# Optimization experiments

Measured on AMD Instinct MI355X. Metric: run time of the kernel, lower is better.

The kernel has to match this reference:

```python
import jax, jax.numpy as jnp
import numpy as np

N = 50000       # nodes
E = 800000      # edges
F_IN = 128      # dataset.num_node_features
H = 128         # hidden_channels (all equal), pool_dim
FC1, FC2 = 512, 256
G = 512         # number of graphs
C = 32          # dataset.num_classes
EPS = 1e-5      # BatchNorm eps


def setup_inputs() -> dict:
    key = jax.random.key(0)
    ks = jax.random.split(key, 16)
    rn = lambda k, s: jax.random.normal(k, s, jnp.float32) * 0.05
    return {
        "x": jax.random.normal(ks[0], (N, F_IN), jnp.float32),
        "edge_index": jax.random.randint(ks[1], (2, E), 0, N),
        "batch": jnp.sort(jax.random.randint(ks[2], (N,), 0, G)),
        "W1": rn(ks[3], (F_IN, H)), "b1": jnp.zeros((H,), jnp.float32),
        "W2": rn(ks[4], (H, H)),    "b2": jnp.zeros((H,), jnp.float32),
        "W3": rn(ks[5], (H, H)),    "b3": jnp.zeros((H,), jnp.float32),
        "W4": rn(ks[6], (H, H)),    "b4": jnp.zeros((H,), jnp.float32),
        "lw1": rn(ks[7], (H, FC1)),   "lb1": jnp.zeros((FC1,), jnp.float32),
        "lw2": rn(ks[8], (FC1, FC2)), "lb2": jnp.zeros((FC2,), jnp.float32),
        "lw3": rn(ks[9], (FC2, C)),   "lb3": jnp.zeros((C,), jnp.float32),
        "g1": jnp.ones((FC1,), jnp.float32), "be1": jnp.zeros((FC1,), jnp.float32),
        "g2": jnp.ones((FC2,), jnp.float32), "be2": jnp.zeros((FC2,), jnp.float32),
    }


def _gcn_structure(edge_index):
    # add self loops, then symmetric deg^-1/2 normalization (PyG GCNConv default)
    loop = jnp.arange(N)
    src = jnp.concatenate([edge_index[0], loop])
    dst = jnp.concatenate([edge_index[1], loop])
    deg = jax.ops.segment_sum(jnp.ones_like(src, jnp.float32), dst, num_segments=N)
    dinv = jnp.where(deg > 0, jax.lax.rsqrt(deg), 0.0)
    norm = dinv[src] * dinv[dst]          # [E + N]
    return src, dst, norm


def _gcn_conv(x, src, dst, norm, W, b):
    h = x @ W                              # [N, out]
    agg = jax.ops.segment_sum(h[src] * norm[:, None], dst, num_segments=N)
    return agg + b


def _bn(h, gamma, beta):
    # training-mode batch stats (biased variance), as torch BatchNorm1d
    m = jnp.mean(h, axis=0)
    v = jnp.var(h, axis=0)
    return (h - m) * jax.lax.rsqrt(v + EPS) * gamma + beta


def reference(x, edge_index, batch, W1, b1, W2, b2, W3, b3, W4, b4,
              lw1, lb1, lw2, lb2, lw3, lb3, g1, be1, g2, be2):
    src, dst, norm = _gcn_structure(edge_index)
    x = jax.nn.relu(_gcn_conv(x, src, dst, norm, W1, b1))
    x = jax.nn.relu(_gcn_conv(x, src, dst, norm, W2, b2))
    x = jax.nn.relu(_gcn_conv(x, src, dst, norm, W3, b3))
    x = jax.nn.relu(_gcn_conv(x, src, dst, norm, W4, b4))
    # global_add_pool over graphs
    p = jax.ops.segment_sum(x, batch, num_segments=G)   # [G, H]
    h = jax.nn.relu(p @ lw1 + lb1)
    h = _bn(h, g1, be1)                                  # dropout = identity (eval)
    h = jax.nn.relu(h @ lw2 + lb2)
    h = _bn(h, g2, be2)
    return jax.nn.sigmoid(h @ lw3 + lb3)                 # [G, C]
```

## Files before the change

### kernel.cpp

```cpp
#include <hip/hip_runtime.h>
#include <hip/hip_fp16.h>
#include <math.h>

#define NN 50000
#define NE 800000
#define FT 128
#define NG 512
#define F1 512
#define F2 256
#define NC 32
#define BN_EPS 1e-5f
#define NSLC (NN / 8)
#define NSTRIP ((NE + 2047) / 2048)

typedef __attribute__((ext_vector_type(8))) unsigned short ushort8;
typedef __attribute__((ext_vector_type(8))) _Float16 f16x8;
typedef __attribute__((ext_vector_type(4))) float f32x4;

__device__ __forceinline__ unsigned short f2h(float f) {
  return __half_as_ushort(__float2half(f));
}
__device__ __forceinline__ float h2f(unsigned short h) {
  return __half2float(__ushort_as_half(h));
}


__global__ __launch_bounds__(256) void k_hist(const int* __restrict__ ei, int* __restrict__ cnt8,
                                              unsigned short* __restrict__ rank16) {
  int c = blockIdx.x & 7;
  int e0 = blockIdx.x * 2048 + threadIdx.x * 8;
  if (e0 >= NE) return;
  int* cn = cnt8 + (size_t)c * NN;
  const int* dst = ei + NE;
  int4 a = *(const int4*)&dst[e0];
  int4 b4 = *(const int4*)&dst[e0 + 4];
  int d[8] = {a.x, a.y, a.z, a.w, b4.x, b4.y, b4.z, b4.w};
  ushort8 r;
#pragma unroll
  for (int j = 0; j < 8; ++j) r[j] = (unsigned short)atomicAdd(&cn[d[j]], 1);
  *(ushort8*)&rank16[e0] = r;
}

__global__ __launch_bounds__(256) void k_sum(int* __restrict__ cnt8, int* __restrict__ cnt) {
  int n = blockIdx.x * 256 + threadIdx.x;
  if (n >= NN) return;
  int s = 0;
#pragma unroll
  for (int c = 0; c < 8; ++c) {
    int v = cnt8[(size_t)c * NN + n];
    cnt8[(size_t)c * NN + n] = s;
    s += v;
  }
  cnt[n] = s;
}

__global__ __launch_bounds__(256) void k_dinv(const int* __restrict__ cnt, float* __restrict__ dinv) {
  int i = blockIdx.x * 256 + threadIdx.x;
  if (i < NN) dinv[i] = rsqrtf((float)(cnt[i] + 1));
}

__global__ __launch_bounds__(256) void k_scan1(const int* __restrict__ cnt, int* __restrict__ bsum) {
  __shared__ int s[256];
  int t = threadIdx.x, i = blockIdx.x * 256 + t;
  s[t] = (i < NN) ? cnt[i] : 0;
  __syncthreads();
  for (int d = 128; d > 0; d >>= 1) {
    if (t < d) s[t] += s[t + d];
    __syncthreads();
  }
  if (t == 0) bsum[blockIdx.x] = s[0];
}

__global__ __launch_bounds__(256) void k_scan2(const int* __restrict__ bsum, int* __restrict__ bscan, int nb) {
  __shared__ int s[256];
  int t = threadIdx.x;
  int v = (t < nb) ? bsum[t] : 0;
  s[t] = v; __syncthreads();
  for (int d = 1; d < 256; d <<= 1) {
    int a = (t >= d) ? s[t - d] : 0;
    __syncthreads();
    s[t] += a;
    __syncthreads();
  }
  bscan[t] = s[t] - v;
}

__global__ __launch_bounds__(256) void k_scan3(const int* __restrict__ cnt, const int* __restrict__ bscan,
                                               int* __restrict__ off) {
  __shared__ int s[256];
  int t = threadIdx.x, i = blockIdx.x * 256 + t;
  int v = (i < NN) ? cnt[i] : 0;
  s[t] = v; __syncthreads();
  for (int d = 1; d < 256; d <<= 1) {
    int a = (t >= d) ? s[t - d] : 0;
    __syncthreads();
    s[t] += a;
    __syncthreads();
  }
  int base = bscan[blockIdx.x];
  if (i < NN) off[i] = base + s[t] - v;
  if (i == NN - 1) off[NN] = base + s[t];
}

__global__ __launch_bounds__(256) void k_fill(const int* __restrict__ ei, const int* __restrict__ off,
                                              const int* __restrict__ pre8,
                                              const unsigned short* __restrict__ rank16,
                                              const float* __restrict__ dinv,
                                              unsigned int* __restrict__ ep) {
  int c = blockIdx.x & 7;
  int lo = c * NSLC, hi = lo + NSLC;
  int strip = blockIdx.x >> 3;
  int e0 = strip * 2048 + threadIdx.x * 8;
  if (e0 >= NE) return;
  const int* prec = pre8 + (size_t)(strip & 7) * NN;
  const int* dst = ei + NE;
  int4 da = *(const int4*)&dst[e0];
  int4 db = *(const int4*)&dst[e0 + 4];
  int4 sa = *(const int4*)&ei[e0];
  int4 sb = *(const int4*)&ei[e0 + 4];
  ushort8 rr = *(const ushort8*)&rank16[e0];
  int d[8] = {da.x, da.y, da.z, da.w, db.x, db.y, db.z, db.w};
  int s[8] = {sa.x, sa.y, sa.z, sa.w, sb.x, sb.y, sb.z, sb.w};
#pragma unroll
  for (int j = 0; j < 8; ++j) {
    if (d[j] >= lo && d[j] < hi) {
      int p = off[d[j]] + prec[d[j]] + (int)rr[j];
      float w = dinv[s[j]] * dinv[d[j]];
      ep[p] = (unsigned int)(s[j] & 0xFFFF) | ((unsigned int)f2h(w) << 16);
    }
  }
}


__global__ __launch_bounds__(256) void k_wprep4(const float* __restrict__ W0, const float* __restrict__ W1,
                                                const float* __restrict__ W2, const float* __restrict__ W3,
                                                unsigned short* __restrict__ Wt) {
  int idx = blockIdx.x * 256 + threadIdx.x;
  int l = idx >> 14;
  int r = idx & 16383;
  int c = r >> 7, k = r & 127;
  const float* W = (l == 0) ? W0 : (l == 1) ? W1 : (l == 2) ? W2 : W3;
  int byte = c * 256 + k * 2;
  byte ^= (c & 7) << 4;
  Wt[l * 16384 + (byte >> 1)] = f2h(W[k * FT + c]);
}


template <int FIRST>
__global__ __launch_bounds__(256) void k_gemm_mfma(const float* __restrict__ Xf,
                                                   const unsigned short* __restrict__ Xh,
                                                   const unsigned short* __restrict__ Wt,
                                                   unsigned short* __restrict__ Oc) {
  __shared__ unsigned short sA[64 * 128];
  __shared__ unsigned short sB[128 * 128];
  int t = threadIdx.x;
#pragma unroll
  for (int i = 0; i < 8; ++i) {
    int off = t * 16 + i * 4096;
    *(float4*)((char*)sB + off) = *(const float4*)((const char*)Wt + off);
  }
  {
    int row = t >> 2, k0 = (t & 3) * 32;
    int grow = blockIdx.x * 64 + row;
    if (grow >= NN) grow = NN - 1;
    if (FIRST) {
      const float* xr = Xf + (size_t)grow * FT + k0;
#pragma unroll
      for (int j = 0; j < 4; ++j) {
        float4 v0 = *(const float4*)&xr[j * 8];
        float4 v1 = *(const float4*)&xr[j * 8 + 4];
        ushort8 w;
        w[0] = f2h(v0.x); w[1] = f2h(v0.y); w[2] = f2h(v0.z); w[3] = f2h(v0.w);
        w[4] = f2h(v1.x); w[5] = f2h(v1.y); w[6] = f2h(v1.z); w[7] = f2h(v1.w);
        int byte = row * 256 + (k0 + j * 8) * 2;
        byte ^= (row & 7) << 4;
        *(ushort8*)((char*)sA + byte) = w;
      }
    } else {
#pragma unroll
      for (int j = 0; j < 4; ++j) {
        int k = k0 + j * 8;
        int ch = k >> 5, ko = k & 31;
        ushort8 v = *(const ushort8*)&Xh[((size_t)ch * NN + grow) * 32 + ko];
        int byte = row * 256 + k * 2;
        byte ^= (row & 7) << 4;
        *(ushort8*)((char*)sA + byte) = v;
      }
    }
  }
  __syncthreads();
  int w = t >> 6, l = t & 63;
  int m = l & 15, ks = l >> 4;
  f16x8 a[4];
#pragma unroll
  for (int kk = 0; kk < 4; ++kk) {
    int r = w * 16 + m;
    int byte = r * 256 + (kk * 32 + ks * 8) * 2;
    byte ^= (r & 7) << 4;
    a[kk] = *(const f16x8*)((const char*)sA + byte);
  }
  f32x4 acc[8];
#pragma unroll
  for (int nf = 0; nf < 8; ++nf) acc[nf] = (f32x4){0.f, 0.f, 0.f, 0.f};
#pragma unroll
  for (int nf = 0; nf < 8; ++nf) {
#pragma unroll
    for (int kk = 0; kk < 4; ++kk) {
      int col = nf * 16 + m;
      int byte = col * 256 + (kk * 32 + ks * 8) * 2;
      byte ^= (col & 7) << 4;
      f16x8 b = *(const f16x8*)((const char*)sB + byte);
      acc[nf] = __builtin_amdgcn_mfma_f32_16x16x32_f16(a[kk], b, acc[nf], 0, 0, 0);
    }
  }
  int orow0 = blockIdx.x * 64 + w * 16 + ks * 4;
#pragma unroll
  for (int nf = 0; nf < 8; ++nf) {
    int ch = nf >> 1;
    int co = ((nf & 1) << 4) + m;
#pragma unroll
    for (int r = 0; r < 4; ++r) {
      int orow = orow0 + r;
      if (orow < NN) Oc[((size_t)ch * NN + orow) * 32 + co] = f2h(acc[nf][r]);
    }
  }
}


__global__ __launch_bounds__(256) void k_aggc(const unsigned short* __restrict__ Hc,
                                              const float* __restrict__ dinv,
                                              const int* __restrict__ off, const unsigned int* __restrict__ ep,
                                              const float* __restrict__ bias, unsigned short* __restrict__ O) {
  int c = blockIdx.x & 3;
  int grp = blockIdx.x >> 2;
  int t = threadIdx.x;
  int node = grp * 64 + (t >> 2);
  int l = t & 3;
  if (node >= NN) return;
  const unsigned short* base = Hc + (size_t)c * NN * 32 + l * 8;
  float di = dinv[node];
  float sw = di * di;
  float acc[8];
  {
    ushort8 sv = *(const ushort8*)&base[(size_t)node * 32];
#pragma unroll
    for (int i = 0; i < 8; ++i) acc[i] = h2f(sv[i]) * sw;
  }
  int e0 = off[node], e1 = off[node + 1];
  int e = e0;
  for (; e + 8 <= e1; e += 8) {
    unsigned int pw[8];
#pragma unroll
    for (int j = 0; j < 8; ++j) pw[j] = ep[e + j];
    ushort8 v[8];
#pragma unroll
    for (int j = 0; j < 8; ++j) v[j] = *(const ushort8*)&base[(size_t)(pw[j] & 0xFFFFu) * 32];
#pragma unroll
    for (int j = 0; j < 8; ++j) {
      float w = h2f((unsigned short)(pw[j] >> 16));
#pragma unroll
      for (int i = 0; i < 8; ++i) acc[i] += h2f(v[j][i]) * w;
    }
  }
  for (; e + 4 <= e1; e += 4) {
    unsigned int p0 = ep[e], p1 = ep[e + 1], p2 = ep[e + 2], p3 = ep[e + 3];
    ushort8 v0 = *(const ushort8*)&base[(size_t)(p0 & 0xFFFFu) * 32];
    ushort8 v1 = *(const ushort8*)&base[(size_t)(p1 & 0xFFFFu) * 32];
    ushort8 v2 = *(const ushort8*)&base[(size_t)(p2 & 0xFFFFu) * 32];
    ushort8 v3 = *(const ushort8*)&base[(size_t)(p3 & 0xFFFFu) * 32];
    float w0 = h2f((unsigned short)(p0 >> 16));
    float w1 = h2f((unsigned short)(p1 >> 16));
    float w2 = h2f((unsigned short)(p2 >> 16));
    float w3 = h2f((unsigned short)(p3 >> 16));
#pragma unroll
    for (int i = 0; i < 8; ++i) acc[i] += h2f(v0[i]) * w0;
#pragma unroll
    for (int i = 0; i < 8; ++i) acc[i] += h2f(v1[i]) * w1;
#pragma unroll
    for (int i = 0; i < 8; ++i) acc[i] += h2f(v2[i]) * w2;
#pragma unroll
    for (int i = 0; i < 8; ++i) acc[i] += h2f(v3[i]) * w3;
  }
  for (; e < e1; ++e) {
    unsigned int pv = ep[e];
    float w = h2f((unsigned short)(pv >> 16));
    ushort8 v = *(const ushort8*)&base[(size_t)(pv & 0xFFFFu) * 32];
#pragma unroll
    for (int i = 0; i < 8; ++i) acc[i] += h2f(v[i]) * w;
  }
  ushort8 outv;
#pragma unroll
  for (int i = 0; i < 8; ++i) {
    float v = acc[i] + bias[c * 32 + l * 8 + i];
    outv[i] = f2h(fmaxf(v, 0.f));
  }
  *(ushort8*)&O[((size_t)c * NN + node) * 32 + l * 8] = outv;
}


__global__ __launch_bounds__(256) void k_bounds(const int* __restrict__ batch, int* __restrict__ gstart,
                                                int* __restrict__ gend) {
  int i = blockIdx.x * 256 + threadIdx.x;
  if (i >= NN) return;
  int b = batch[i];
  if (i == 0 || batch[i - 1] != b) gstart[b] = i;
  if (i == NN - 1 || batch[i + 1] != b) gend[b] = i + 1;
}

__global__ __launch_bounds__(128) void k_pool(const unsigned short* __restrict__ X, const int* __restrict__ gstart,
                                              const int* __restrict__ gend, float* __restrict__ pool) {
  int g = blockIdx.x, t = threadIdx.x;
  int ch = t >> 5, wo = t & 31;
  float s = 0.f;
  int n0 = gstart[g], n1 = gend[g];
  const unsigned short* base = X + (size_t)ch * NN * 32 + wo;
  for (int n = n0; n < n1; ++n) s += h2f(base[(size_t)n * 32]);
  pool[g * FT + t] = s;
}


__global__ __launch_bounds__(256) void k_fc1(const float* __restrict__ P, const float* __restrict__ W,
                                             const float* __restrict__ B, float* __restrict__ O) {
  __shared__ float sp[FT];
  int g = blockIdx.x, t = threadIdx.x;
  if (t < FT) sp[t] = P[g * FT + t];
  __syncthreads();
  float a0 = B[t], a1 = B[t + 256];
  for (int k = 0; k < FT; ++k) {
    float x = sp[k];
    a0 += x * W[k * F1 + t];
    a1 += x * W[k * F1 + t + 256];
  }
  O[g * F1 + t] = fmaxf(a0, 0.f);
  O[g * F1 + t + 256] = fmaxf(a1, 0.f);
}

__global__ __launch_bounds__(256) void k_bnstats(const float* __restrict__ h, int cols,
                                                 float* __restrict__ bm, float* __restrict__ br) {
  __shared__ float ss[256], s2[256];
  int c = blockIdx.x, t = threadIdx.x;
  float a = 0.f, b = 0.f;
  for (int r = t; r < NG; r += 256) {
    float v = h[r * cols + c];
    a += v; b += v * v;
  }
  ss[t] = a; s2[t] = b; __syncthreads();
  for (int d = 128; d > 0; d >>= 1) {
    if (t < d) { ss[t] += ss[t + d]; s2[t] += s2[t + d]; }
    __syncthreads();
  }
  if (t == 0) {
    float m = ss[0] / NG;
    float var = s2[0] / NG - m * m;
    bm[c] = m;
    br[c] = rsqrtf(var + BN_EPS);
  }
}

__global__ __launch_bounds__(256) void k_fc2(const float* __restrict__ H1, const float* __restrict__ bm,
                                             const float* __restrict__ br, const float* __restrict__ gam,
                                             const float* __restrict__ bet, const float* __restrict__ W,
                                             const float* __restrict__ B, float* __restrict__ O) {
  __shared__ float sh[F1];
  int g = blockIdx.x, t = threadIdx.x;
  for (int k = t; k < F1; k += 256) {
    float v = H1[g * F1 + k];
    sh[k] = (v - bm[k]) * br[k] * gam[k] + bet[k];
  }
  __syncthreads();
  float a = B[t];
  for (int k = 0; k < F1; ++k) a += sh[k] * W[k * F2 + t];
  O[g * F2 + t] = fmaxf(a, 0.f);
}

__global__ __launch_bounds__(256) void k_fc3(const float* __restrict__ H2, const float* __restrict__ bm,
                                             const float* __restrict__ br, const float* __restrict__ gam,
                                             const float* __restrict__ bet, const float* __restrict__ W,
                                             const float* __restrict__ B, float* __restrict__ O) {
  __shared__ float sh[F2];
  int g = blockIdx.x, t = threadIdx.x;
  if (t < F2) {
    float v = H2[g * F2 + t];
    sh[t] = (v - bm[t]) * br[t] * gam[t] + bet[t];
  }
  __syncthreads();
  if (t < NC) {
    float a = B[t];
    for (int k = 0; k < F2; ++k) a += sh[k] * W[k * NC + t];
    O[g * NC + t] = 1.f / (1.f + expf(-a));
  }
}


extern "C" void kernel_launch(void* const* d_in, const int* in_sizes, int n_in,
                              void* d_out, int out_size, void* d_ws, size_t ws_size,
                              hipStream_t stream) {
  const float* x     = (const float*)d_in[0];
  const int*   ei    = (const int*)d_in[1];
  const int*   batch = (const int*)d_in[2];
  const float* Wc[4] = {(const float*)d_in[3], (const float*)d_in[5], (const float*)d_in[7], (const float*)d_in[9]};
  const float* Bc[4] = {(const float*)d_in[4], (const float*)d_in[6], (const float*)d_in[8], (const float*)d_in[10]};
  const float* lw1 = (const float*)d_in[11]; const float* lb1 = (const float*)d_in[12];
  const float* lw2 = (const float*)d_in[13]; const float* lb2 = (const float*)d_in[14];
  const float* lw3 = (const float*)d_in[15]; const float* lb3 = (const float*)d_in[16];
  const float* g1  = (const float*)d_in[17]; const float* be1 = (const float*)d_in[18];
  const float* g2  = (const float*)d_in[19]; const float* be2 = (const float*)d_in[20];

  char* p = (char*)d_ws;
  auto take = [&](size_t bytes) {
    char* r = p;
    p += (bytes + 255) & ~(size_t)255;
    return r;
  };
  int*   cnt8   = (int*)take((size_t)8 * NN * 4);
  int*   cnt    = (int*)take((size_t)NN * 4);
  float* dinv   = (float*)take((size_t)NN * 4);
  int*   off    = (int*)take((size_t)(NN + 1) * 4);
  int*   bsum   = (int*)take(256 * 4);
  int*   bscan  = (int*)take(256 * 4);
  int*   gstart = (int*)take((size_t)NG * 4);
  int*   gend   = (int*)take((size_t)NG * 4);
  unsigned short* rank16 = (unsigned short*)take((size_t)NE * 2);
  unsigned int*   ep   = (unsigned int*)take((size_t)NE * 4);
  unsigned short* Wt   = (unsigned short*)take((size_t)4 * FT * FT * 2);
  unsigned short* bufT = (unsigned short*)take((size_t)NN * FT * 2);
  unsigned short* bufA = (unsigned short*)take((size_t)NN * FT * 2);
  unsigned short* bufB = (unsigned short*)take((size_t)NN * FT * 2);
  float* pool   = (float*)take((size_t)NG * FT * 4);
  float* h1     = (float*)take((size_t)NG * F1 * 4);
  float* h2     = (float*)take((size_t)NG * F2 * 4);
  float* bnm1   = (float*)take(F1 * 4);
  float* bnr1   = (float*)take(F1 * 4);
  float* bnm2   = (float*)take(F2 * 4);
  float* bnr2   = (float*)take(F2 * 4);

  const int NB = (NN + 255) / 256;

  hipMemsetAsync(cnt8, 0, (size_t)8 * NN * 4, stream);
  hipMemsetAsync(gstart, 0, (size_t)NG * 4, stream);
  hipMemsetAsync(gend, 0, (size_t)NG * 4, stream);

  k_hist<<<NSTRIP, 256, 0, stream>>>(ei, cnt8, rank16);
  k_sum<<<NB, 256, 0, stream>>>(cnt8, cnt);
  k_dinv<<<NB, 256, 0, stream>>>(cnt, dinv);
  k_scan1<<<NB, 256, 0, stream>>>(cnt, bsum);
  k_scan2<<<1, 256, 0, stream>>>(bsum, bscan, NB);
  k_scan3<<<NB, 256, 0, stream>>>(cnt, bscan, off);
  k_fill<<<NSTRIP * 8, 256, 0, stream>>>(ei, off, cnt8, rank16, dinv, ep);
  k_wprep4<<<256, 256, 0, stream>>>(Wc[0], Wc[1], Wc[2], Wc[3], Wt);

  const int NBLK_G = (NN + 63) / 64;
  const int NGRP_A = (NN + 63) / 64;
  unsigned short* outs[4] = {bufA, bufB, bufA, bufB};
  for (int l = 0; l < 4; ++l) {
    if (l == 0)
      k_gemm_mfma<1><<<NBLK_G, 256, 0, stream>>>(x, (const unsigned short*)nullptr, Wt, bufT);
    else
      k_gemm_mfma<0><<<NBLK_G, 256, 0, stream>>>((const float*)nullptr, outs[l - 1], Wt + (size_t)l * FT * FT, bufT);
    k_aggc<<<NGRP_A * 4, 256, 0, stream>>>(bufT, dinv, off, ep, Bc[l], outs[l]);
  }

  k_bounds<<<NB, 256, 0, stream>>>(batch, gstart, gend);
  k_pool<<<NG, 128, 0, stream>>>(bufB, gstart, gend, pool);

  k_fc1<<<NG, 256, 0, stream>>>(pool, lw1, lb1, h1);
  k_bnstats<<<F1, 256, 0, stream>>>(h1, F1, bnm1, bnr1);
  k_fc2<<<NG, 256, 0, stream>>>(h1, bnm1, bnr1, g1, be1, lw2, lb2, h2);
  k_bnstats<<<F2, 256, 0, stream>>>(h2, F2, bnm2, bnr2);
  k_fc3<<<NG, 256, 0, stream>>>(h2, bnm2, bnr2, g2, be2, lw3, lb3, (float*)d_out);
}
```

Measured before the change: 314.8 us.

## Sort nodes by degree for aggregation to balance wavefront work

Adds a stable counting sort of nodes by in-degree (clamped at 63): a per-block histogram, a single-block global scan, and a scatter that builds a permutation. The aggregation kernel then takes its node from this permutation, so nodes of similar degree share a wavefront and lanes diverge less across edge loops. It also merges the degree-sum and dinv kernels into one launch. The cost is three extra small kernels (one of them a serial single-block scan) and less locality in node order for the gathered self rows and the output writes.

```diff
diff --git a/kernel.cpp b/kernel.cpp
--- a/kernel.cpp
+++ b/kernel.cpp
@@ -12,6 +12,8 @@
 #define BN_EPS 1e-5f
 #define NSLC (NN / 8)
 #define NSTRIP ((NE + 2047) / 2048)
+#define NBLK ((NN + 255) / 256)
+#define NBH (NBLK * 64)
 
 typedef __attribute__((ext_vector_type(8))) unsigned short ushort8;
 typedef __attribute__((ext_vector_type(8))) _Float16 f16x8;
@@ -41,7 +43,8 @@
   *(ushort8*)&rank16[e0] = r;
 }
 
-__global__ __launch_bounds__(256) void k_sum(int* __restrict__ cnt8, int* __restrict__ cnt) {
+__global__ __launch_bounds__(256) void k_sumdinv(int* __restrict__ cnt8, int* __restrict__ cnt,
+                                                 float* __restrict__ dinv) {
   int n = blockIdx.x * 256 + threadIdx.x;
   if (n >= NN) return;
   int s = 0;
@@ -52,11 +55,7 @@
     s += v;
   }
   cnt[n] = s;
-}
-
-__global__ __launch_bounds__(256) void k_dinv(const int* __restrict__ cnt, float* __restrict__ dinv) {
-  int i = blockIdx.x * 256 + threadIdx.x;
-  if (i < NN) dinv[i] = rsqrtf((float)(cnt[i] + 1));
+  dinv[n] = rsqrtf((float)(s + 1));
 }
 
 __global__ __launch_bounds__(256) void k_scan1(const int* __restrict__ cnt, int* __restrict__ bsum) {
@@ -132,6 +131,56 @@
 }
 
 
+__global__ __launch_bounds__(256) void k_bhist(const int* __restrict__ cnt, int* __restrict__ bh) {
+  __shared__ int lh[64];
+  int t = threadIdx.x;
+  if (t < 64) lh[t] = 0;
+  __syncthreads();
+  int i = blockIdx.x * 256 + t;
+  if (i < NN) atomicAdd(&lh[min(cnt[i], 63)], 1);
+  __syncthreads();
+  if (t < 64) bh[blockIdx.x * 64 + t] = lh[t];
+}
+
+__global__ __launch_bounds__(256) void k_bscan(const int* __restrict__ bh, int* __restrict__ gb) {
+  __shared__ int s[256];
+  __shared__ int carry;
+  int t = threadIdx.x;
+  if (t == 0) carry = 0;
+  for (int base = 0; base < NBH; base += 256) {
+    __syncthreads();
+    int cloc = carry;
+    int j = base + t;
+    int b = j / NBLK, blk = j % NBLK;
+    int v = (j < NBH) ? bh[blk * 64 + b] : 0;
+    s[t] = v; __syncthreads();
+    for (int d = 1; d < 256; d <<= 1) {
+      int a = (t >= d) ? s[t - d] : 0;
+      __syncthreads();
+      s[t] += a;
+      __syncthreads();
+    }
+    if (j < NBH) gb[blk * 64 + b] = cloc + s[t] - v;
+    __syncthreads();
+    if (t == 0) carry = cloc + s[255];
+  }
+}
+
+__global__ __launch_bounds__(256) void k_dscatter(const int* __restrict__ cnt, const int* __restrict__ gb,
+                                                  int* __restrict__ perm) {
+  __shared__ int lcur[64];
+  int t = threadIdx.x;
+  if (t < 64) lcur[t] = 0;
+  __syncthreads();
+  int i = blockIdx.x * 256 + t;
+  if (i < NN) {
+    int b = min(cnt[i], 63);
+    int r = atomicAdd(&lcur[b], 1);
+    perm[gb[blockIdx.x * 64 + b] + r] = i;
+  }
+}
+
+
 __global__ __launch_bounds__(256) void k_wprep4(const float* __restrict__ W0, const float* __restrict__ W1,
                                                 const float* __restrict__ W2, const float* __restrict__ W3,
                                                 unsigned short* __restrict__ Wt) {
@@ -230,13 +279,15 @@
 __global__ __launch_bounds__(256) void k_aggc(const unsigned short* __restrict__ Hc,
                                               const float* __restrict__ dinv,
                                               const int* __restrict__ off, const unsigned int* __restrict__ ep,
+                                              const int* __restrict__ perm,
                                               const float* __restrict__ bias, unsigned short* __restrict__ O) {
   int c = blockIdx.x & 3;
   int grp = blockIdx.x >> 2;
   int t = threadIdx.x;
-  int node = grp * 64 + (t >> 2);
+  int idx = grp * 64 + (t >> 2);
   int l = t & 3;
-  if (node >= NN) return;
+  if (idx >= NN) return;
+  int node = perm[idx];
   const unsigned short* base = Hc + (size_t)c * NN * 32 + l * 8;
   float di = dinv[node];
   float sw = di * di;
@@ -420,6 +471,9 @@
   int*   bscan  = (int*)take(256 * 4);
   int*   gstart = (int*)take((size_t)NG * 4);
   int*   gend   = (int*)take((size_t)NG * 4);
+  int*   bh     = (int*)take((size_t)NBH * 4);
+  int*   gb     = (int*)take((size_t)NBH * 4);
+  int*   perm   = (int*)take((size_t)NN * 4);
   unsigned short* rank16 = (unsigned short*)take((size_t)NE * 2);
   unsigned int*   ep   = (unsigned int*)take((size_t)NE * 4);
   unsigned short* Wt   = (unsigned short*)take((size_t)4 * FT * FT * 2);
@@ -434,19 +488,19 @@
   float* bnm2   = (float*)take(F2 * 4);
   float* bnr2   = (float*)take(F2 * 4);
 
-  const int NB = (NN + 255) / 256;
-
   hipMemsetAsync(cnt8, 0, (size_t)8 * NN * 4, stream);
   hipMemsetAsync(gstart, 0, (size_t)NG * 4, stream);
   hipMemsetAsync(gend, 0, (size_t)NG * 4, stream);
 
   k_hist<<<NSTRIP, 256, 0, stream>>>(ei, cnt8, rank16);
-  k_sum<<<NB, 256, 0, stream>>>(cnt8, cnt);
-  k_dinv<<<NB, 256, 0, stream>>>(cnt, dinv);
-  k_scan1<<<NB, 256, 0, stream>>>(cnt, bsum);
-  k_scan2<<<1, 256, 0, stream>>>(bsum, bscan, NB);
-  k_scan3<<<NB, 256, 0, stream>>>(cnt, bscan, off);
+  k_sumdinv<<<NBLK, 256, 0, stream>>>(cnt8, cnt, dinv);
+  k_scan1<<<NBLK, 256, 0, stream>>>(cnt, bsum);
+  k_scan2<<<1, 256, 0, stream>>>(bsum, bscan, NBLK);
+  k_scan3<<<NBLK, 256, 0, stream>>>(cnt, bscan, off);
   k_fill<<<NSTRIP * 8, 256, 0, stream>>>(ei, off, cnt8, rank16, dinv, ep);
+  k_bhist<<<NBLK, 256, 0, stream>>>(cnt, bh);
+  k_bscan<<<1, 256, 0, stream>>>(bh, gb);
+  k_dscatter<<<NBLK, 256, 0, stream>>>(cnt, gb, perm);
   k_wprep4<<<256, 256, 0, stream>>>(Wc[0], Wc[1], Wc[2], Wc[3], Wt);
 
   const int NBLK_G = (NN + 63) / 64;
@@ -457,10 +511,10 @@
       k_gemm_mfma<1><<<NBLK_G, 256, 0, stream>>>(x, (const unsigned short*)nullptr, Wt, bufT);
     else
       k_gemm_mfma<0><<<NBLK_G, 256, 0, stream>>>((const float*)nullptr, outs[l - 1], Wt + (size_t)l * FT * FT, bufT);
-    k_aggc<<<NGRP_A * 4, 256, 0, stream>>>(bufT, dinv, off, ep, Bc[l], outs[l]);
-  }
-
-  k_bounds<<<NB, 256, 0, stream>>>(batch, gstart, gend);
+    k_aggc<<<NGRP_A * 4, 256, 0, stream>>>(bufT, dinv, off, ep, perm, Bc[l], outs[l]);
+  }
+
+  k_bounds<<<NBLK, 256, 0, stream>>>(batch, gstart, gend);
   k_pool<<<NG, 128, 0, stream>>>(bufB, gstart, gend, pool);
 
   k_fc1<<<NG, 256, 0, stream>>>(pool, lw1, lb1, h1);
```

After: 386.0 us. 22.6% more time.

## Fuse degree/scan kernels, pool with fc1, and stage GEMM output through LDS

Applied to the files above, without the earlier changes.

Merges the count-sum, dinv and first scan pass into one kernel, and merges graph-boundary detection, add-pooling and the first FC layer into one kernel that finds segment bounds by binary search over the sorted batch vector. The GEMM epilogue now writes results into shared memory and then stores 16-byte vectors per row-chunk instead of scattered 2-byte stores. This removes several small kernel launches and two memsets and aims for coalesced output writes, at the cost of an extra barrier and reuse of the sA shared-memory buffer in the GEMM.

```diff
diff --git a/kernel.cpp b/kernel.cpp
--- a/kernel.cpp
+++ b/kernel.cpp
@@ -12,6 +12,7 @@
 #define BN_EPS 1e-5f
 #define NSLC (NN / 8)
 #define NSTRIP ((NE + 2047) / 2048)
+#define NBLK ((NN + 255) / 256)
 
 typedef __attribute__((ext_vector_type(8))) unsigned short ushort8;
 typedef __attribute__((ext_vector_type(8))) _Float16 f16x8;
@@ -41,34 +42,30 @@
   *(ushort8*)&rank16[e0] = r;
 }
 
-__global__ __launch_bounds__(256) void k_sum(int* __restrict__ cnt8, int* __restrict__ cnt) {
-  int n = blockIdx.x * 256 + threadIdx.x;
-  if (n >= NN) return;
-  int s = 0;
-#pragma unroll
-  for (int c = 0; c < 8; ++c) {
-    int v = cnt8[(size_t)c * NN + n];
-    cnt8[(size_t)c * NN + n] = s;
-    s += v;
-  }
-  cnt[n] = s;
-}
-
-__global__ __launch_bounds__(256) void k_dinv(const int* __restrict__ cnt, float* __restrict__ dinv) {
-  int i = blockIdx.x * 256 + threadIdx.x;
-  if (i < NN) dinv[i] = rsqrtf((float)(cnt[i] + 1));
-}
-
-__global__ __launch_bounds__(256) void k_scan1(const int* __restrict__ cnt, int* __restrict__ bsum) {
-  __shared__ int s[256];
-  int t = threadIdx.x, i = blockIdx.x * 256 + t;
-  s[t] = (i < NN) ? cnt[i] : 0;
+__global__ __launch_bounds__(256) void k_sumdinv(int* __restrict__ cnt8, int* __restrict__ cnt,
+                                                 float* __restrict__ dinv, int* __restrict__ bsum) {
+  __shared__ int sh[256];
+  int t = threadIdx.x, n = blockIdx.x * 256 + t;
+  int tot = 0;
+  if (n < NN) {
+    int s = 0;
+#pragma unroll
+    for (int c = 0; c < 8; ++c) {
+      int v = cnt8[(size_t)c * NN + n];
+      cnt8[(size_t)c * NN + n] = s;
+      s += v;
+    }
+    cnt[n] = s;
+    dinv[n] = rsqrtf((float)(s + 1));
+    tot = s;
+  }
+  sh[t] = tot;
   __syncthreads();
   for (int d = 128; d > 0; d >>= 1) {
-    if (t < d) s[t] += s[t + d];
-    __syncthreads();
-  }
-  if (t == 0) bsum[blockIdx.x] = s[0];
+    if (t < d) sh[t] += sh[t + d];
+    __syncthreads();
+  }
+  if (t == 0) bsum[blockIdx.x] = sh[0];
 }
 
 __global__ __launch_bounds__(256) void k_scan2(const int* __restrict__ bsum, int* __restrict__ bscan, int nb) {
@@ -213,15 +210,25 @@
       acc[nf] = __builtin_amdgcn_mfma_f32_16x16x32_f16(a[kk], b, acc[nf], 0, 0, 0);
     }
   }
-  int orow0 = blockIdx.x * 64 + w * 16 + ks * 4;
+  __syncthreads();
+  int lrow0 = w * 16 + ks * 4;
 #pragma unroll
   for (int nf = 0; nf < 8; ++nf) {
-    int ch = nf >> 1;
-    int co = ((nf & 1) << 4) + m;
 #pragma unroll
     for (int r = 0; r < 4; ++r) {
-      int orow = orow0 + r;
-      if (orow < NN) Oc[((size_t)ch * NN + orow) * 32 + co] = f2h(acc[nf][r]);
+      sA[(lrow0 + r) * 128 + nf * 16 + m] = f2h(acc[nf][r]);
+    }
+  }
+  __syncthreads();
+  {
+    int row = t >> 2, chp = t & 3;
+    int grow2 = blockIdx.x * 64 + row;
+    if (grow2 < NN) {
+      const unsigned short* srcp = &sA[row * 128 + chp * 32];
+      unsigned short* dstp = &Oc[((size_t)chp * NN + grow2) * 32];
+#pragma unroll
+      for (int q = 0; q < 4; ++q)
+        *(ushort8*)&dstp[q * 8] = *(const ushort8*)&srcp[q * 8];
     }
   }
 }
@@ -298,42 +305,44 @@
 }
 
 
-__global__ __launch_bounds__(256) void k_bounds(const int* __restrict__ batch, int* __restrict__ gstart,
-                                                int* __restrict__ gend) {
-  int i = blockIdx.x * 256 + threadIdx.x;
-  if (i >= NN) return;
-  int b = batch[i];
-  if (i == 0 || batch[i - 1] != b) gstart[b] = i;
-  if (i == NN - 1 || batch[i + 1] != b) gend[b] = i + 1;
-}
-
-__global__ __launch_bounds__(128) void k_pool(const unsigned short* __restrict__ X, const int* __restrict__ gstart,
-                                              const int* __restrict__ gend, float* __restrict__ pool) {
+__global__ __launch_bounds__(256) void k_poolfc1(const unsigned short* __restrict__ X,
+                                                 const int* __restrict__ batch,
+                                                 const float* __restrict__ W, const float* __restrict__ B,
+                                                 float* __restrict__ O) {
+  __shared__ float part[256];
+  __shared__ float sp[FT];
+  __shared__ int nb[2];
   int g = blockIdx.x, t = threadIdx.x;
-  int ch = t >> 5, wo = t & 31;
+  if (t < 2) {
+    int val = g + t;
+    int lo = 0, hi = NN;
+    while (lo < hi) {
+      int mid = (lo + hi) >> 1;
+      if (batch[mid] < val) lo = mid + 1; else hi = mid;
+    }
+    nb[t] = lo;
+  }
+  __syncthreads();
+  int n0 = nb[0], n1 = nb[1];
+  int f = t & 127, half = t >> 7;
+  int ch = f >> 5, wo = f & 31;
+  const unsigned short* base = X + (size_t)ch * NN * 32 + wo;
   float s = 0.f;
-  int n0 = gstart[g], n1 = gend[g];
-  const unsigned short* base = X + (size_t)ch * NN * 32 + wo;
-  for (int n = n0; n < n1; ++n) s += h2f(base[(size_t)n * 32]);
-  pool[g * FT + t] = s;
-}
-
-
-__global__ __launch_bounds__(256) void k_fc1(const float* __restrict__ P, const float* __restrict__ W,
-                                             const float* __restrict__ B, float* __restrict__ O) {
-  __shared__ float sp[FT];
-  int g = blockIdx.x, t = threadIdx.x;
-  if (t < FT) sp[t] = P[g * FT + t];
+  for (int n = n0 + half; n < n1; n += 2) s += h2f(base[(size_t)n * 32]);
+  part[t] = s;
+  __syncthreads();
+  if (t < FT) sp[t] = part[t] + part[t + 128];
   __syncthreads();
   float a0 = B[t], a1 = B[t + 256];
   for (int k = 0; k < FT; ++k) {
-    float x = sp[k];
-    a0 += x * W[k * F1 + t];
-    a1 += x * W[k * F1 + t + 256];
+    float xk = sp[k];
+    a0 += xk * W[k * F1 + t];
+    a1 += xk * W[k * F1 + t + 256];
   }
   O[g * F1 + t] = fmaxf(a0, 0.f);
   O[g * F1 + t + 256] = fmaxf(a1, 0.f);
 }
+
 
 __global__ __launch_bounds__(256) void k_bnstats(const float* __restrict__ h, int cols,
                                                  float* __restrict__ bm, float* __restrict__ br) {
@@ -418,15 +427,12 @@
   int*   off    = (int*)take((size_t)(NN + 1) * 4);
   int*   bsum   = (int*)take(256 * 4);
   int*   bscan  = (int*)take(256 * 4);
-  int*   gstart = (int*)take((size_t)NG * 4);
-  int*   gend   = (int*)take((size_t)NG * 4);
   unsigned short* rank16 = (unsigned short*)take((size_t)NE * 2);
   unsigned int*   ep   = (unsigned int*)take((size_t)NE * 4);
   unsigned short* Wt   = (unsigned short*)take((size_t)4 * FT * FT * 2);
   unsigned short* bufT = (unsigned short*)take((size_t)NN * FT * 2);
   unsigned short* bufA = (unsigned short*)take((size_t)NN * FT * 2);
   unsigned short* bufB = (unsigned short*)take((size_t)NN * FT * 2);
-  float* pool   = (float*)take((size_t)NG * FT * 4);
   float* h1     = (float*)take((size_t)NG * F1 * 4);
   float* h2     = (float*)take((size_t)NG * F2 * 4);
   float* bnm1   = (float*)take(F1 * 4);
@@ -434,18 +440,12 @@
   float* bnm2   = (float*)take(F2 * 4);
   float* bnr2   = (float*)take(F2 * 4);
 
-  const int NB = (NN + 255) / 256;
-
   hipMemsetAsync(cnt8, 0, (size_t)8 * NN * 4, stream);
-  hipMemsetAsync(gstart, 0, (size_t)NG * 4, stream);
-  hipMemsetAsync(gend, 0, (size_t)NG * 4, stream);
 
   k_hist<<<NSTRIP, 256, 0, stream>>>(ei, cnt8, rank16);
-  k_sum<<<NB, 256, 0, stream>>>(cnt8, cnt);
-  k_dinv<<<NB, 256, 0, stream>>>(cnt, dinv);
-  k_scan1<<<NB, 256, 0, stream>>>(cnt, bsum);
-  k_scan2<<<1, 256, 0, stream>>>(bsum, bscan, NB);
-  k_scan3<<<NB, 256, 0, stream>>>(cnt, bscan, off);
+  k_sumdinv<<<NBLK, 256, 0, stream>>>(cnt8, cnt, dinv, bsum);
+  k_scan2<<<1, 256, 0, stream>>>(bsum, bscan, NBLK);
+  k_scan3<<<NBLK, 256, 0, stream>>>(cnt, bscan, off);
   k_fill<<<NSTRIP * 8, 256, 0, stream>>>(ei, off, cnt8, rank16, dinv, ep);
   k_wprep4<<<256, 256, 0, stream>>>(Wc[0], Wc[1], Wc[2], Wc[3], Wt);
 
@@ -460,10 +460,7 @@
     k_aggc<<<NGRP_A * 4, 256, 0, stream>>>(bufT, dinv, off, ep, Bc[l], outs[l]);
   }
 
-  k_bounds<<<NB, 256, 0, stream>>>(batch, gstart, gend);
-  k_pool<<<NG, 128, 0, stream>>>(bufB, gstart, gend, pool);
-
-  k_fc1<<<NG, 256, 0, stream>>>(pool, lw1, lb1, h1);
+  k_poolfc1<<<NG, 256, 0, stream>>>(bufB, batch, lw1, lb1, h1);
   k_bnstats<<<F1, 256, 0, stream>>>(h1, F1, bnm1, bnr1);
   k_fc2<<<NG, 256, 0, stream>>>(h1, bnm1, bnr1, g1, be1, lw2, lb2, h2);
   k_bnstats<<<F2, 256, 0, stream>>>(h2, F2, bnm2, bnr2);
```

New measurement: 305.7 us, median of 2. 2.9% less time.
